# Kernel optimization log

Hardware: AMD Instinct MI355X
Metric: run time of the kernel (lower is better)

Reference implementation:

```python
import jax, jax.numpy as jnp
import numpy as np

# dims from VideoTokenizerConfig defaults + chosen video shape
B, T, IH, IW, C = 2, 16, 224, 224, 3
TP, PS, D, DFF, L, NH, K = 4, 16, 512, 2048, 6, 8, 8192
Tp, Hp, Wp = T // TP, IH // PS, IW // PS   # 4, 14, 14
S = Tp * Hp * Wp                           # 784 tokens
PIN = TP * PS * PS * C                     # 3072 patch elements
COMMIT = 0.25


def _ln(x, s, b):
    m = x.mean(-1, keepdims=True)
    v = ((x - m) ** 2).mean(-1, keepdims=True)
    return (x - m) / jnp.sqrt(v + 1e-6) * s + b


def _mha(x, Wqkv, bqkv, Wo, bo):
    b_, s_, d_ = x.shape
    hd = d_ // NH
    q = (x @ Wqkv[0] + bqkv[0]).reshape(b_, s_, NH, hd)
    k = (x @ Wqkv[1] + bqkv[1]).reshape(b_, s_, NH, hd)
    v = (x @ Wqkv[2] + bqkv[2]).reshape(b_, s_, NH, hd)
    att = jax.nn.softmax(jnp.einsum('bqhd,bkhd->bhqk', q, k) / jnp.sqrt(jnp.float32(hd)), axis=-1)
    o = jnp.einsum('bhqk,bkhd->bqhd', att, v).reshape(b_, s_, d_)
    return o @ Wo + bo


def _blocks(z, ln1s, ln1b, Wqkv, bqkv, Wo, bo, ln2s, ln2b, W1, b1, W2, b2):
    for i in range(L):  # small fixed layer count
        z = z + _mha(_ln(z, ln1s[i], ln1b[i]), Wqkv[i], bqkv[i], Wo[i], bo[i])
        h = jax.nn.gelu(_ln(z, ln2s[i], ln2b[i]) @ W1[i] + b1[i])
        z = z + h @ W2[i] + b2[i]
    return z


def _forward(video, e_patch_W, e_patch_b, e_pos_t, e_pos_h, e_pos_w,
             e_ln1_s, e_ln1_b, e_Wqkv, e_bqkv, e_Wo, e_bo, e_ln2_s, e_ln2_b,
             e_W1, e_b1, e_W2, e_b2, e_lnf_s, e_lnf_b, e_cb_W, e_cb_b,
             codebook,
             d_cb_W, d_cb_b, d_pos_t, d_pos_h, d_pos_w,
             d_ln1_s, d_ln1_b, d_Wqkv, d_bqkv, d_Wo, d_bo, d_ln2_s, d_ln2_b,
             d_W1, d_b1, d_W2, d_b2, d_lnf_s, d_lnf_b, d_px_W, d_px_b):
    # ---- encoder: 3D patchify ----
    v = video.reshape(B, Tp, TP, Hp, PS, Wp, PS, C)
    v = v.transpose(0, 1, 3, 5, 2, 4, 6, 7).reshape(B, Tp, Hp, Wp, PIN)
    z = v @ e_patch_W + e_patch_b
    z = z + e_pos_t + e_pos_h + e_pos_w
    z = z.reshape(B, S, D)
    z = _blocks(z, e_ln1_s, e_ln1_b, e_Wqkv, e_bqkv, e_Wo, e_bo,
                e_ln2_s, e_ln2_b, e_W1, e_b1, e_W2, e_b2)
    z = _ln(z, e_lnf_s, e_lnf_b)
    z_e = z @ e_cb_W + e_cb_b                      # [B,S,D]
    # ---- VQ quantize ----
    flat = z_e.reshape(-1, D)                      # [B*S, D]
    d2 = (flat ** 2).sum(1, keepdims=True) + (codebook ** 2).sum(1) - 2.0 * flat @ codebook.T
    idx = jnp.argmin(d2, axis=1)                   # [B*S]
    z_q = codebook[idx].reshape(z_e.shape)
    commit = jnp.mean((jax.lax.stop_gradient(z_q) - z_e) ** 2)
    cb_loss = jnp.mean((z_q - jax.lax.stop_gradient(z_e)) ** 2)
    z_q = z_e + jax.lax.stop_gradient(z_q - z_e)   # straight-through
    counts = jnp.zeros((K,), flat.dtype).at[idx].add(1.0)
    p = counts / idx.shape[0]                      # == mean(one_hot, axis=0)
    perplexity = jnp.exp(-jnp.sum(p * jnp.log(p + 1e-10)))
    # ---- decoder ----
    zd = z_q.reshape(B, Tp, Hp, Wp, D) @ d_cb_W + d_cb_b
    zd = zd + d_pos_t + d_pos_h + d_pos_w
    zd = zd.reshape(B, S, D)
    zd = _blocks(zd, d_ln1_s, d_ln1_b, d_Wqkv, d_bqkv, d_Wo, d_bo,
                 d_ln2_s, d_ln2_b, d_W1, d_b1, d_W2, d_b2)
    zd = _ln(zd, d_lnf_s, d_lnf_b)
    px = zd.reshape(B, Tp, Hp, Wp, D) @ d_px_W + d_px_b
    px = px.reshape(B, Tp, Hp, Wp, TP, PS, PS, C)
    recon = px.transpose(0, 1, 4, 2, 5, 3, 6, 7).reshape(B, T, IH, IW, C)
    return recon, idx.reshape(B, Tp, Hp, Wp), commit, cb_loss, perplexity


def setup_inputs() -> dict:
    key = jax.random.key(0)
    ks = iter(jax.random.split(key, 48))
    def nrm(shape, s=0.02):
        return (s * jax.random.normal(next(ks), shape)).astype(jnp.float32)
    z = lambda shape: jnp.zeros(shape, jnp.float32)
    o = lambda shape: jnp.ones(shape, jnp.float32)
    inp = {}
    inp['video'] = jax.random.normal(next(ks), (B, T, IH, IW, C), jnp.float32)
    # encoder params
    inp['e_patch_W'] = nrm((PIN, D)); inp['e_patch_b'] = z((D,))
    inp['e_pos_t'] = nrm((1, Tp, 1, 1, D)); inp['e_pos_h'] = nrm((1, 1, Hp, 1, D)); inp['e_pos_w'] = nrm((1, 1, 1, Wp, D))
    inp['e_ln1_s'] = o((L, D)); inp['e_ln1_b'] = z((L, D))
    inp['e_Wqkv'] = nrm((L, 3, D, D)); inp['e_bqkv'] = z((L, 3, D))
    inp['e_Wo'] = nrm((L, D, D)); inp['e_bo'] = z((L, D))
    inp['e_ln2_s'] = o((L, D)); inp['e_ln2_b'] = z((L, D))
    inp['e_W1'] = nrm((L, D, DFF)); inp['e_b1'] = z((L, DFF))
    inp['e_W2'] = nrm((L, DFF, D)); inp['e_b2'] = z((L, D))
    inp['e_lnf_s'] = o((D,)); inp['e_lnf_b'] = z((D,))
    inp['e_cb_W'] = nrm((D, D)); inp['e_cb_b'] = z((D,))
    inp['codebook'] = nrm((K, D))
    # decoder params
    inp['d_cb_W'] = nrm((D, D)); inp['d_cb_b'] = z((D,))
    inp['d_pos_t'] = nrm((1, Tp, 1, 1, D)); inp['d_pos_h'] = nrm((1, 1, Hp, 1, D)); inp['d_pos_w'] = nrm((1, 1, 1, Wp, D))
    inp['d_ln1_s'] = o((L, D)); inp['d_ln1_b'] = z((L, D))
    inp['d_Wqkv'] = nrm((L, 3, D, D)); inp['d_bqkv'] = z((L, 3, D))
    inp['d_Wo'] = nrm((L, D, D)); inp['d_bo'] = z((L, D))
    inp['d_ln2_s'] = o((L, D)); inp['d_ln2_b'] = z((L, D))
    inp['d_W1'] = nrm((L, D, DFF)); inp['d_b1'] = z((L, DFF))
    inp['d_W2'] = nrm((L, DFF, D)); inp['d_b2'] = z((L, D))
    inp['d_lnf_s'] = o((D,)); inp['d_lnf_b'] = z((D,))
    inp['d_px_W'] = nrm((D, PIN)); inp['d_px_b'] = z((PIN,))
    return inp


def reference(video, e_patch_W, e_patch_b, e_pos_t, e_pos_h, e_pos_w,
              e_ln1_s, e_ln1_b, e_Wqkv, e_bqkv, e_Wo, e_bo, e_ln2_s, e_ln2_b,
              e_W1, e_b1, e_W2, e_b2, e_lnf_s, e_lnf_b, e_cb_W, e_cb_b,
              codebook,
              d_cb_W, d_cb_b, d_pos_t, d_pos_h, d_pos_w,
              d_ln1_s, d_ln1_b, d_Wqkv, d_bqkv, d_Wo, d_bo, d_ln2_s, d_ln2_b,
              d_W1, d_b1, d_W2, d_b2, d_lnf_s, d_lnf_b, d_px_W, d_px_b):
    return _forward(video, e_patch_W, e_patch_b, e_pos_t, e_pos_h, e_pos_w,
                    e_ln1_s, e_ln1_b, e_Wqkv, e_bqkv, e_Wo, e_bo, e_ln2_s, e_ln2_b,
                    e_W1, e_b1, e_W2, e_b2, e_lnf_s, e_lnf_b, e_cb_W, e_cb_b,
                    codebook,
                    d_cb_W, d_cb_b, d_pos_t, d_pos_h, d_pos_w,
                    d_ln1_s, d_ln1_b, d_Wqkv, d_bqkv, d_Wo, d_bo, d_ln2_s, d_ln2_b,
                    d_W1, d_b1, d_W2, d_b2, d_lnf_s, d_lnf_b, d_px_W, d_px_b)
```

## Files before the change

### kernel.cpp

```cpp
#include <hip/hip_runtime.h>
#include <math.h>

#define Bq    2
#define Dq    512
#define DFFq  2048
#define Lq    6
#define NHq   8
#define HDq   64
#define Kq    8192
#define Sq    784
#define PINq  3072
#define TOKq  1568
#define RECN  4816896L

#define OFF_BIG  0L
#define SZ_BIG   12845056L
#define OFF_Z    (OFF_BIG + SZ_BIG)
#define OFF_XLN  (OFF_Z    + 802816L)
#define OFF_QKV  (OFF_XLN  + 802816L)
#define OFF_ATTO (OFF_QKV  + 2408448L)
#define OFF_H    (OFF_ATTO + 802816L)
#define OFF_ZE   (OFF_H    + 3211264L)
#define OFF_ZQ   (OFF_ZE   + 802816L)
#define OFF_CN   (OFF_ZQ   + 802816L)
#define OFF_IDX  (OFF_CN   + 8192L)
#define OFF_CNT  (OFF_IDX  + 1568L)
#define OFF_PART (OFF_CNT  + 8192L)
#define OFF_MIN  (OFF_PART + 1568L)
#define OFF_END  (OFF_MIN  + 3136L)

#define CEXT 802816L

typedef short bf16x8 __attribute__((ext_vector_type(8)));
typedef float f32x4  __attribute__((ext_vector_type(4)));
typedef unsigned short u16;
typedef unsigned long long u64;

#define XLO 802816L
#define QLO 2408448L
#define ALO 802816L
#define HLO 3211264L
#define PLO 4816896L
#define ZLO 802816L
#define CBLO 4194304L

__device__ __forceinline__ float wave_sum(float v) {
    #pragma unroll
    for (int o = 32; o; o >>= 1) v += __shfl_xor(v, o);
    return v;
}
__device__ __forceinline__ float gelu_f(float x) {
    float u = 0.7978845608028654f * (x + 0.044715f * x * x * x);
    float a = fabsf(u);
    float t = __expf(-2.0f * a);
    float th = (1.0f - t) / (1.0f + t);
    th = copysignf(th, u);
    return 0.5f * x * (1.0f + th);
}
__device__ __forceinline__ void split_f32(float x, u16& h, u16& l) {
    unsigned u = __float_as_uint(x);
    unsigned t = u + 0x7fffu + ((u >> 16) & 1u);
    h = (u16)(t >> 16);
    float r = x - __uint_as_float((t >> 16) << 16);
    l = (u16)(__float_as_uint(r) >> 16);
}
__device__ __forceinline__ void gload16(const u16* g, u16* l) {
    __builtin_amdgcn_global_load_lds(
        (const __attribute__((address_space(1))) void*)g,
        (__attribute__((address_space(3))) void*)l,
        16, 0, 0);
}

__global__ __launch_bounds__(256)
void wconv_t(const float* __restrict__ W, int ldw, int Kd,
             u16* __restrict__ WT, long loT, long soW, long soT)
{
    __shared__ u16 Lh[32][33], Ll[32][33];
    const float* Wp = W + (long)blockIdx.z * soW;
    u16* Tp = WT + (long)blockIdx.z * soT;
    int k0 = blockIdx.x << 5, n0 = blockIdx.y << 5;
    int t = threadIdx.x;
    int r = t >> 3, c4 = (t & 7) << 2;
    float4 v = *(const float4*)(Wp + (long)(k0 + r) * ldw + n0 + c4);
    u16 h, l;
    split_f32(v.x, h, l); Lh[c4+0][r] = h; Ll[c4+0][r] = l;
    split_f32(v.y, h, l); Lh[c4+1][r] = h; Ll[c4+1][r] = l;
    split_f32(v.z, h, l); Lh[c4+2][r] = h; Ll[c4+2][r] = l;
    split_f32(v.w, h, l); Lh[c4+3][r] = h; Ll[c4+3][r] = l;
    __syncthreads();
    int n = t >> 3, kc = (t & 7) << 2;
    u16* dst = Tp + (long)(n0 + n) * Kd + k0 + kc;
    u16 oh[4] = {Lh[n][kc], Lh[n][kc+1], Lh[n][kc+2], Lh[n][kc+3]};
    u16 ol[4] = {Ll[n][kc], Ll[n][kc+1], Ll[n][kc+2], Ll[n][kc+3]};
    *(uint2*)dst = *(uint2*)oh;
    *(uint2*)(dst + loT) = *(uint2*)ol;
}

__global__ __launch_bounds__(256)
void wconv4(const float* __restrict__ Wqkv, const float* __restrict__ Wo,
            const float* __restrict__ W1, const float* __restrict__ W2,
            u16* __restrict__ dst)
{
    __shared__ u16 Lh[32][33], Ll[32][33];
    int id = blockIdx.x;
    const float* W; int ldw, Kd, kblk, nblk; u16* Tp; long loT;
    if (id < 768) {
        int z = id >> 8, rid = id & 255;
        kblk = rid & 15; nblk = rid >> 4;
        W = Wqkv + (long)z * 262144; ldw = 512; Kd = 512;
        Tp = dst + (long)z * 262144; loT = 786432;
    } else if (id < 1024) {
        int rid = id - 768; kblk = rid & 15; nblk = rid >> 4;
        W = Wo; ldw = 512; Kd = 512; Tp = dst + 1572864; loT = 262144;
    } else if (id < 2048) {
        int rid = id - 1024; kblk = rid & 15; nblk = rid >> 4;
        W = W1; ldw = 2048; Kd = 512; Tp = dst + 2097152; loT = 1048576;
    } else {
        int rid = id - 2048; kblk = rid & 63; nblk = rid >> 6;
        W = W2; ldw = 512; Kd = 2048; Tp = dst + 4194304; loT = 1048576;
    }
    int k0 = kblk << 5, n0 = nblk << 5;
    int t = threadIdx.x;
    int r = t >> 3, c4 = (t & 7) << 2;
    float4 v = *(const float4*)(W + (long)(k0 + r) * ldw + n0 + c4);
    u16 h, l;
    split_f32(v.x, h, l); Lh[c4+0][r] = h; Ll[c4+0][r] = l;
    split_f32(v.y, h, l); Lh[c4+1][r] = h; Ll[c4+1][r] = l;
    split_f32(v.z, h, l); Lh[c4+2][r] = h; Ll[c4+2][r] = l;
    split_f32(v.w, h, l); Lh[c4+3][r] = h; Ll[c4+3][r] = l;
    __syncthreads();
    int n = t >> 3, kc = (t & 7) << 2;
    u16* d = Tp + (long)(n0 + n) * Kd + k0 + kc;
    u16 oh[4] = {Lh[n][kc], Lh[n][kc+1], Lh[n][kc+2], Lh[n][kc+3]};
    u16 ol[4] = {Ll[n][kc], Ll[n][kc+1], Ll[n][kc+2], Ll[n][kc+3]};
    *(uint2*)d = *(uint2*)oh;
    *(uint2*)(d + loT) = *(uint2*)ol;
}

__global__ __launch_bounds__(256)
void splitp(const float* __restrict__ X, u16* __restrict__ Y, long lo, long n4)
{
    long i = (long)blockIdx.x * 256 + threadIdx.x;
    if (i >= n4) return;
    float4 v = *(const float4*)(X + i * 4);
    u16 h[4], l[4];
    split_f32(v.x, h[0], l[0]); split_f32(v.y, h[1], l[1]);
    split_f32(v.z, h[2], l[2]); split_f32(v.w, h[3], l[3]);
    *(uint2*)(Y + i * 4) = *(uint2*)h;
    *(uint2*)(Y + lo + i * 4) = *(uint2*)l;
}

template<int MATH, int LV>
__global__ __launch_bounds__(256)
void gemm_bb(const u16* __restrict__ A, long rsA, long loA, long soA, long siA,
             const u16* __restrict__ B, long rsB, long loB, long soB, long siB,
             const float* __restrict__ bias, long siBias,
             const float* __restrict__ extra,
             float* __restrict__ Cf, int ldc, long soC, long siC,
             u16* __restrict__ Cb, int rsC, long loC,
             float* __restrict__ part, long pstride,
             int M, int N, int K, float alpha,
             int bdiv, int ksplit, int klen, int gx)
{
    constexpr int OFF_BH = (LV >= 2) ? 8192 : 4096;
    __shared__ u16 SH[LV == 3 ? 16384 : (LV == 2 ? 12288 : 8192)];
    const int zb2 = blockIdx.z;
    const int zk = zb2 % ksplit, zb = zb2 / ksplit;
    const int zo = zb / bdiv, zi = zb - zo * bdiv;
    A += zo * soA + zi * siA;
    B += zo * soB + zi * siB;
    const float* bi = bias ? bias + zi * siBias : nullptr;

    const int nwg = gridDim.x;
    int orig = blockIdx.x;
    int qq = nwg >> 3, rr = nwg & 7;
    int xcd = orig & 7, sidx = orig >> 3;
    int wgid = (xcd < rr ? xcd * (qq + 1) : rr * (qq + 1) + (xcd - rr) * qq) + sidx;
    const int m0 = (wgid % gx) << 6, n0 = (wgid / gx) << 6;

    const int t = threadIdx.x;
    const int kbeg = zk * klen;
    int kend = kbeg + klen; if (kend > K) kend = K;

    const int w = t >> 6, lane = t & 63;
    const int wm = w >> 1, wn = w & 1;
    const int l15 = lane & 15, g = lane >> 4;
    const int wq = w << 9;

    const int csrc = ((t & 3) + ((t >> 3) & 7)) & 3;
    int arow = m0 + (t >> 2); if (arow > M - 1) arow = M - 1;
    const u16* Apr = A + (long)arow * rsA + (csrc << 3);
    const u16* Bpr = B + (long)(n0 + (t >> 2)) * rsB + (csrc << 3);

    f32x4 acc[2][2] = {};

    for (int k0 = kbeg; k0 < kend; k0 += 64) {
        gload16(Apr + k0,            &SH[wq]);
        if (LV >= 2) gload16(Apr + k0 + loA,      &SH[4096 + wq]);
        gload16(Bpr + k0,            &SH[OFF_BH + wq]);
        if (LV == 3) gload16(Bpr + k0 + loB, &SH[12288 + wq]);
        gload16(Apr + k0 + 32,       &SH[2048 + wq]);
        if (LV >= 2) gload16(Apr + k0 + 32 + loA, &SH[4096 + 2048 + wq]);
        gload16(Bpr + k0 + 32,       &SH[OFF_BH + 2048 + wq]);
        if (LV == 3) gload16(Bpr + k0 + 32 + loB, &SH[12288 + 2048 + wq]);
        __syncthreads();

        #pragma unroll
        for (int sub = 0; sub < 2; ++sub) {
            const int so = sub << 11;
            bf16x8 ah[2], al2[2], bh2[2], bl2[2];
            #pragma unroll
            for (int mi = 0; mi < 2; ++mi) {
                int row = (wm << 5) + (mi << 4) + l15;
                int off = (row << 5) + (((g - (row >> 1)) & 3) << 3);
                ah[mi]  = *(const bf16x8*)&SH[so + off];
                if (LV >= 2) al2[mi] = *(const bf16x8*)&SH[4096 + so + off];
            }
            #pragma unroll
            for (int ni = 0; ni < 2; ++ni) {
                int row = (wn << 5) + (ni << 4) + l15;
                int off = (row << 5) + (((g - (row >> 1)) & 3) << 3);
                bh2[ni] = *(const bf16x8*)&SH[OFF_BH + so + off];
                if (LV == 3) bl2[ni] = *(const bf16x8*)&SH[12288 + so + off];
            }
            #pragma unroll
            for (int mi = 0; mi < 2; ++mi)
                #pragma unroll
                for (int ni = 0; ni < 2; ++ni) {
                    acc[mi][ni] = __builtin_amdgcn_mfma_f32_16x16x32_bf16(ah[mi], bh2[ni], acc[mi][ni], 0, 0, 0);
                    if (LV == 3) acc[mi][ni] = __builtin_amdgcn_mfma_f32_16x16x32_bf16(ah[mi], bl2[ni], acc[mi][ni], 0, 0, 0);
                    if (LV >= 2) acc[mi][ni] = __builtin_amdgcn_mfma_f32_16x16x32_bf16(al2[mi], bh2[ni], acc[mi][ni], 0, 0, 0);
                }
        }
        __syncthreads();
    }

    if (ksplit > 1) {
        float* P = part + (long)zk * pstride + zo * soC + zi * siC;
        #pragma unroll
        for (int mi = 0; mi < 2; ++mi)
            #pragma unroll
            for (int ni = 0; ni < 2; ++ni) {
                int gn = n0 + (wn << 5) + (ni << 4) + l15;
                if (gn >= N) continue;
                int gmb = m0 + (wm << 5) + (mi << 4) + (g << 2);
                #pragma unroll
                for (int r = 0; r < 4; ++r) {
                    int gm = gmb + r;
                    if (gm < M) P[(long)gm * ldc + gn] = acc[mi][ni][r];
                }
            }
        return;
    }
    if (MATH == 0) {
        float* Co = Cf + zo * soC + zi * siC;
        #pragma unroll
        for (int mi = 0; mi < 2; ++mi)
            #pragma unroll
            for (int ni = 0; ni < 2; ++ni) {
                int gn = n0 + (wn << 5) + (ni << 4) + l15;
                if (gn >= N) continue;
                int gmb = m0 + (wm << 5) + (mi << 4) + (g << 2);
                #pragma unroll
                for (int r = 0; r < 4; ++r) {
                    int gm = gmb + r;
                    if (gm >= M) continue;
                    Co[(long)gm * ldc + gn] = alpha * acc[mi][ni][r] + (bi ? bi[gn] : 0.0f);
                }
            }
    } else if (MATH == 5) {
        u64* mb = (u64*)Cf;
        #pragma unroll
        for (int mi = 0; mi < 2; ++mi) {
            #pragma unroll
            for (int r = 0; r < 4; ++r) {
                u64 best = 0xFFFFFFFFFFFFFFFFULL;
                #pragma unroll
                for (int ni = 0; ni < 2; ++ni) {
                    int gn = n0 + (wn << 5) + (ni << 4) + l15;
                    float v = extra[gn] - 2.0f * acc[mi][ni][r];
                    unsigned ub = __float_as_uint(v);
                    ub = ub ^ ((ub >> 31) ? 0xFFFFFFFFu : 0x80000000u);
                    u64 pk = ((u64)ub << 32) | (unsigned)gn;
                    best = pk < best ? pk : best;
                }
                #pragma unroll
                for (int sft = 1; sft <= 8; sft <<= 1) {
                    u64 o = __shfl_xor(best, sft);
                    best = o < best ? o : best;
                }
                if (l15 == 0) {
                    int gm = m0 + (wm << 5) + (mi << 4) + (g << 2) + r;
                    if (gm < M) atomicMin(&mb[gm], best);
                }
            }
        }
    } else {
        u16* Cu = Cb + zo * soC + zi * siC;
        #pragma unroll
        for (int mi = 0; mi < 2; ++mi)
            #pragma unroll
            for (int ni = 0; ni < 2; ++ni) {
                int gn = n0 + (wn << 5) + (ni << 4) + l15;
                if (gn >= N) continue;
                int gmb = m0 + (wm << 5) + (mi << 4) + (g << 2);
                #pragma unroll
                for (int r = 0; r < 4; ++r) {
                    int gm = gmb + r;
                    if (gm >= M) continue;
                    float v = acc[mi][ni][r] + bi[gn];
                    if (MATH == 2) v = gelu_f(v);
                    u16 h, l; split_f32(v, h, l);
                    Cu[(long)gm * rsC + gn] = h;
                    Cu[(long)gm * rsC + gn + loC] = l;
                }
            }
    }
}

#define KP 72
#define VP 40
#define CHR 196
template<bool X2>
__global__ __launch_bounds__(256)
void flash_kernel(const u16* __restrict__ qkv, float* __restrict__ O4, float* __restrict__ ML)
{
    __shared__ u16 Kh[32 * KP], Kl[32 * KP];
    __shared__ u16 Vh[64 * VP], Vl[64 * VP];
    __shared__ u16 Ph[64 * VP], Pl[64 * VP];

    const int qb = blockIdx.x, bh = blockIdx.y, ch = blockIdx.z;
    const int b = bh >> 3, h = bh & 7;
    const int jbeg = ch * CHR, jend = jbeg + CHR;
    const int t = threadIdx.x, w = t >> 6, lane = t & 63;
    const int l15 = lane & 15, g = lane >> 4;
    const long base = (long)b * 784 * 1536;
    const u16* Qg = qkv + base + h * 64;
    const u16* Kg = qkv + base + 512 + h * 64;
    const u16* Vg = qkv + base + 1024 + h * 64;

    const int q0 = qb << 6;
    int qr = q0 + w * 16 + l15; if (qr > 783) qr = 783;
    const u16* Qp = Qg + (long)qr * 1536 + g * 8;
    bf16x8 qh[2], ql[2];
    qh[0] = *(const bf16x8*)(Qp);
    qh[1] = *(const bf16x8*)(Qp + 32);
    ql[0] = *(const bf16x8*)(Qp + QLO);
    ql[1] = *(const bf16x8*)(Qp + QLO + 32);

    f32x4 O[4] = {};
    float m_[4] = {-1e30f, -1e30f, -1e30f, -1e30f};
    float l_[4] = {};

    const int srow = t >> 3, sc = (t & 7) << 3;

    for (int j0 = jbeg; j0 < jend; j0 += 32) {
        {
            int jr = j0 + srow;
            if (jr < jend) {
                const u16* Kp = Kg + (long)jr * 1536 + sc;
                *(uint4*)&Kh[srow * KP + sc] = *(const uint4*)(Kp);
                if (!X2) *(uint4*)&Kl[srow * KP + sc] = *(const uint4*)(Kp + QLO);
                const u16* Vp = Vg + (long)jr * 1536 + sc;
                u16 th[8], tl[8];
                *(uint4*)th = *(const uint4*)Vp;
                if (!X2) *(uint4*)tl = *(const uint4*)(Vp + QLO);
                #pragma unroll
                for (int e = 0; e < 8; ++e) {
                    Vh[(sc + e) * VP + srow] = th[e];
                    if (!X2) Vl[(sc + e) * VP + srow] = tl[e];
                }
            } else {
                uint4 zz = {0, 0, 0, 0};
                *(uint4*)&Kh[srow * KP + sc] = zz;
                if (!X2) *(uint4*)&Kl[srow * KP + sc] = zz;
                #pragma unroll
                for (int e = 0; e < 8; ++e) {
                    Vh[(sc + e) * VP + srow] = 0;
                    if (!X2) Vl[(sc + e) * VP + srow] = 0;
                }
            }
        }
        __syncthreads();

        f32x4 S[2] = {};
        #pragma unroll
        for (int f = 0; f < 2; ++f) {
            #pragma unroll
            for (int ks = 0; ks < 2; ++ks) {
                bf16x8 kh = *(const bf16x8*)&Kh[(f * 16 + l15) * KP + ks * 32 + g * 8];
                S[f] = __builtin_amdgcn_mfma_f32_16x16x32_bf16(qh[ks], kh, S[f], 0, 0, 0);
                if (!X2) {
                    bf16x8 kl = *(const bf16x8*)&Kl[(f * 16 + l15) * KP + ks * 32 + g * 8];
                    S[f] = __builtin_amdgcn_mfma_f32_16x16x32_bf16(qh[ks], kl, S[f], 0, 0, 0);
                }
                S[f] = __builtin_amdgcn_mfma_f32_16x16x32_bf16(ql[ks], kh, S[f], 0, 0, 0);
            }
        }

        float p[2][4];
        #pragma unroll
        for (int f = 0; f < 2; ++f) {
            bool ok = (j0 + f * 16 + l15) < jend;
            #pragma unroll
            for (int r = 0; r < 4; ++r)
                p[f][r] = ok ? S[f][r] * 0.125f : -1e30f;
        }
        #pragma unroll
        for (int r = 0; r < 4; ++r) {
            float pm = fmaxf(p[0][r], p[1][r]);
            pm = fmaxf(pm, __shfl_xor(pm, 1)); pm = fmaxf(pm, __shfl_xor(pm, 2));
            pm = fmaxf(pm, __shfl_xor(pm, 4)); pm = fmaxf(pm, __shfl_xor(pm, 8));
            float mn = fmaxf(m_[r], pm);
            float scl = __expf(m_[r] - mn);
            float rs = 0.f;
            #pragma unroll
            for (int f = 0; f < 2; ++f) { float e = __expf(p[f][r] - mn); p[f][r] = e; rs += e; }
            rs += __shfl_xor(rs, 1); rs += __shfl_xor(rs, 2);
            rs += __shfl_xor(rs, 4); rs += __shfl_xor(rs, 8);
            l_[r] = l_[r] * scl + rs;
            m_[r] = mn;
            O[0][r] *= scl; O[1][r] *= scl; O[2][r] *= scl; O[3][r] *= scl;
        }

        #pragma unroll
        for (int f = 0; f < 2; ++f)
            #pragma unroll
            for (int r = 0; r < 4; ++r) {
                u16 hh, ll; split_f32(p[f][r], hh, ll);
                int row = w * 16 + g * 4 + r;
                Ph[row * VP + f * 16 + l15] = hh;
                Pl[row * VP + f * 16 + l15] = ll;
            }

        bf16x8 pah = *(const bf16x8*)&Ph[(w * 16 + l15) * VP + g * 8];
        bf16x8 pal = *(const bf16x8*)&Pl[(w * 16 + l15) * VP + g * 8];
        #pragma unroll
        for (int f = 0; f < 4; ++f) {
            bf16x8 vh = *(const bf16x8*)&Vh[(f * 16 + l15) * VP + g * 8];
            O[f] = __builtin_amdgcn_mfma_f32_16x16x32_bf16(pah, vh, O[f], 0, 0, 0);
            O[f] = __builtin_amdgcn_mfma_f32_16x16x32_bf16(pal, vh, O[f], 0, 0, 0);
            if (!X2) {
                bf16x8 vl = *(const bf16x8*)&Vl[(f * 16 + l15) * VP + g * 8];
                O[f] = __builtin_amdgcn_mfma_f32_16x16x32_bf16(pah, vl, O[f], 0, 0, 0);
            }
        }
        __syncthreads();
    }

    #pragma unroll
    for (int r = 0; r < 4; ++r) {
        int q = q0 + w * 16 + g * 4 + r;
        if (q >= 784) continue;
        long rowi = ((long)ch * 16 + bh) * 784 + q;
        if (l15 == 0) { ML[rowi * 2] = m_[r]; ML[rowi * 2 + 1] = l_[r]; }
        #pragma unroll
        for (int f = 0; f < 4; ++f)
            O4[rowi * 64 + f * 16 + l15] = O[f][r];
    }
}

__global__ __launch_bounds__(256)
void flash_combine(const float* __restrict__ O4, const float* __restrict__ ML,
                   u16* __restrict__ atto)
{
    int wave = threadIdx.x >> 6, lane = threadIdx.x & 63;
    int row = (blockIdx.x << 2) + wave;
    int bh = row / 784, q = row - bh * 784;
    int b = bh >> 3, h = bh & 7;
    float mm[4], ll[4];
    float M = -1e30f;
    #pragma unroll
    for (int c = 0; c < 4; ++c) {
        long ri = ((long)c * 16 + bh) * 784 + q;
        mm[c] = ML[ri * 2]; ll[c] = ML[ri * 2 + 1];
        M = fmaxf(M, mm[c]);
    }
    float L = 0.f, sc[4];
    #pragma unroll
    for (int c = 0; c < 4; ++c) { sc[c] = __expf(mm[c] - M); L += sc[c] * ll[c]; }
    float o = 0.f;
    #pragma unroll
    for (int c = 0; c < 4; ++c)
        o += O4[(((long)c * 16 + bh) * 784 + q) * 64 + lane] * sc[c];
    o /= L;
    u16 hh, lo2; split_f32(o, hh, lo2);
    long off = ((long)b * 784 + q) * 512 + h * 64 + lane;
    atto[off] = hh; atto[off + ALO] = lo2;
}

template<int MATH>
__global__ __launch_bounds__(256)
void reduce_k(const float* __restrict__ part, long pstride, int ks,
              const float* __restrict__ bias, int ldc,
              float* __restrict__ Cf, u16* __restrict__ Cb, long loC, long total)
{
    long i = (long)blockIdx.x * 256 + threadIdx.x;
    if (i >= total) return;
    float s = 0.f;
    for (int k = 0; k < ks; ++k) s += part[(long)k * pstride + i];
    int col = (int)(i % ldc);
    float v = s + (bias ? bias[col] : 0.0f);
    if (MATH == 3) { Cf[i] = v; u16 h, l; split_f32(v, h, l); Cb[i] = h; Cb[i + loC] = l; }
    else { float g = gelu_f(v); u16 h, l; split_f32(g, h, l); Cb[i] = h; Cb[i + loC] = l; }
}

__global__ __launch_bounds__(256)
void redln(const float* __restrict__ part, long pstride, int ks,
           const float* __restrict__ bias,
           float* __restrict__ z,
           const float* __restrict__ s, const float* __restrict__ b,
           u16* __restrict__ y, long lo)
{
    int wave = threadIdx.x >> 6, lane = threadIdx.x & 63;
    int row = (blockIdx.x << 2) + wave;
    int c0 = lane << 3;
    long base = (long)row * 512 + c0;
    float a[8] = {};
    for (int k = 0; k < ks; ++k) {
        const float* p = part + (long)k * pstride + base;
        float4 p0 = *(const float4*)p, p1 = *(const float4*)(p + 4);
        a[0]+=p0.x; a[1]+=p0.y; a[2]+=p0.z; a[3]+=p0.w;
        a[4]+=p1.x; a[5]+=p1.y; a[6]+=p1.z; a[7]+=p1.w;
    }
    float4 b0 = *(const float4*)(bias + c0), b1 = *(const float4*)(bias + c0 + 4);
    a[0]+=b0.x; a[1]+=b0.y; a[2]+=b0.z; a[3]+=b0.w;
    a[4]+=b1.x; a[5]+=b1.y; a[6]+=b1.z; a[7]+=b1.w;
    float4 z0 = *(const float4*)(z + base), z1 = *(const float4*)(z + base + 4);
    float v[8] = { z0.x+a[0], z0.y+a[1], z0.z+a[2], z0.w+a[3],
                   z1.x+a[4], z1.y+a[5], z1.z+a[6], z1.w+a[7] };
    float4 o0, o1;
    o0.x=v[0]; o0.y=v[1]; o0.z=v[2]; o0.w=v[3];
    o1.x=v[4]; o1.y=v[5]; o1.z=v[6]; o1.w=v[7];
    *(float4*)(z + base) = o0; *(float4*)(z + base + 4) = o1;
    float sum = v[0]+v[1]+v[2]+v[3]+v[4]+v[5]+v[6]+v[7];
    sum = wave_sum(sum);
    float m = sum * (1.0f / 512.0f);
    float var = 0.f;
    float d[8];
    #pragma unroll
    for (int j = 0; j < 8; ++j) { d[j] = v[j] - m; var += d[j]*d[j]; }
    var = wave_sum(var);
    float rstd = 1.0f / sqrtf(var * (1.0f / 512.0f) + 1e-6f);
    u16 hh[8], ll[8];
    #pragma unroll
    for (int j = 0; j < 8; ++j)
        split_f32(d[j] * rstd * s[c0+j] + b[c0+j], hh[j], ll[j]);
    *(uint4*)(y + base) = *(uint4*)hh;
    *(uint4*)(y + lo + base) = *(uint4*)ll;
}

__global__ __launch_bounds__(256)
void redposln(const float* __restrict__ part, long pstride, int ks,
              const float* __restrict__ bias,
              const float* __restrict__ pt, const float* __restrict__ ph,
              const float* __restrict__ pw,
              float* __restrict__ z,
              const float* __restrict__ s, const float* __restrict__ b,
              u16* __restrict__ y, long lo)
{
    int wave = threadIdx.x >> 6, lane = threadIdx.x & 63;
    int row = (blockIdx.x << 2) + wave;
    int c0 = lane << 3;
    long base = (long)row * 512 + c0;
    int r = row % 784;
    int wp = r % 14, hh2 = (r / 14) % 14, tp = r / 196;
    float v[8] = {};
    for (int k = 0; k < ks; ++k) {
        const float* p = part + (long)k * pstride + base;
        float4 p0 = *(const float4*)p, p1 = *(const float4*)(p + 4);
        v[0]+=p0.x; v[1]+=p0.y; v[2]+=p0.z; v[3]+=p0.w;
        v[4]+=p1.x; v[5]+=p1.y; v[6]+=p1.z; v[7]+=p1.w;
    }
    const float* ptp = pt + tp * 512 + c0;
    const float* php = ph + hh2 * 512 + c0;
    const float* pwp = pw + wp * 512 + c0;
    #pragma unroll
    for (int j = 0; j < 8; ++j) v[j] += bias[c0+j] + ptp[j] + php[j] + pwp[j];
    float4 o0, o1;
    o0.x=v[0]; o0.y=v[1]; o0.z=v[2]; o0.w=v[3];
    o1.x=v[4]; o1.y=v[5]; o1.z=v[6]; o1.w=v[7];
    *(float4*)(z + base) = o0; *(float4*)(z + base + 4) = o1;
    float sum = v[0]+v[1]+v[2]+v[3]+v[4]+v[5]+v[6]+v[7];
    sum = wave_sum(sum);
    float m = sum * (1.0f / 512.0f);
    float var = 0.f; float d[8];
    #pragma unroll
    for (int j = 0; j < 8; ++j) { d[j] = v[j] - m; var += d[j]*d[j]; }
    var = wave_sum(var);
    float rstd = 1.0f / sqrtf(var * (1.0f / 512.0f) + 1e-6f);
    u16 hh[8], ll[8];
    #pragma unroll
    for (int j = 0; j < 8; ++j)
        split_f32(d[j] * rstd * s[c0+j] + b[c0+j], hh[j], ll[j]);
    *(uint4*)(y + base) = *(uint4*)hh;
    *(uint4*)(y + lo + base) = *(uint4*)ll;
}

__global__ __launch_bounds__(256)
void cnorm_kernel(const float* __restrict__ cb, float* __restrict__ cn)
{
    int wave = threadIdx.x >> 6, lane = threadIdx.x & 63;
    int row = (blockIdx.x << 2) + wave;
    if (row >= Kq) return;
    const float* cr = cb + (long)row * Dq;
    float4 v0 = *(const float4*)(cr + (lane << 2));
    float4 v1 = *(const float4*)(cr + 256 + (lane << 2));
    float ss = v0.x*v0.x+v0.y*v0.y+v0.z*v0.z+v0.w*v0.w
             + v1.x*v1.x+v1.y*v1.y+v1.z*v1.z+v1.w*v1.w;
    ss = wave_sum(ss);
    if (lane == 0) cn[row] = ss;
}

__global__ void patchify_kernel(const float* __restrict__ video, u16* __restrict__ patches)
{
    long i = (long)blockIdx.x * 256 + threadIdx.x;
    if (i >= (long)TOKq * PINq) return;
    int row = (int)(i / PINq), col = (int)(i - (long)row * PINq);
    int c = col % 3; int q = col / 3;
    int pw = q & 15; q >>= 4;
    int ph = q & 15; int tpin = q >> 4;
    int wp = row % 14; int r2 = row / 14;
    int hp = r2 % 14; r2 /= 14;
    int tp = r2 & 3; int b = r2 >> 2;
    int tt = tp * 4 + tpin;
    int ih = hp * 16 + ph, iw = wp * 16 + pw;
    float v = video[(((long)(b * 16 + tt) * 224 + ih) * 224 + iw) * 3 + c];
    u16 h, l; split_f32(v, h, l);
    patches[i] = h; patches[PLO + i] = l;
}

__global__ void unpatchify_kernel(const float* __restrict__ px, float* __restrict__ out)
{
    long o = (long)blockIdx.x * 256 + threadIdx.x;
    if (o >= RECN) return;
    int c = (int)(o % 3); long r = o / 3;
    int iw = (int)(r % 224); r /= 224;
    int ih = (int)(r % 224); r /= 224;
    int tt = (int)(r % 16); int b = (int)(r / 16);
    int tp = tt >> 2, tpin = tt & 3;
    int hp = ih >> 4, ph = ih & 15;
    int wp = iw >> 4, pw = iw & 15;
    long prow = ((long)(b * 4 + tp) * 14 + hp) * 14 + wp;
    int pcol = ((tpin * 16 + ph) * 16 + pw) * 3 + c;
    out[o] = px[prow * PINq + pcol];
}

__global__ __launch_bounds__(256)
void zq_kernel(const float* __restrict__ cb, const u64* __restrict__ minb,
               const float* __restrict__ ze, u16* __restrict__ zqp, long lo,
               float* __restrict__ part, float* __restrict__ counts,
               float* __restrict__ out_idx)
{
    int tok = blockIdx.x;
    int id = (int)(minb[tok] & 0xFFFFFFFFULL);
    const float* c = cb + (long)id * Dq;
    const float* z = ze + (long)tok * Dq;
    float ss = 0.f;
    for (int d = threadIdx.x; d < Dq; d += 256) {
        float cv = c[d];
        u16 h, l; split_f32(cv, h, l);
        zqp[(long)tok * Dq + d] = h;
        zqp[lo + (long)tok * Dq + d] = l;
        float df = cv - z[d];
        ss += df * df;
    }
    float wsum = wave_sum(ss);
    __shared__ float sw[4];
    if ((threadIdx.x & 63) == 0) sw[threadIdx.x >> 6] = wsum;
    __syncthreads();
    if (threadIdx.x == 0) {
        part[tok] = sw[0] + sw[1] + sw[2] + sw[3];
        atomicAdd(&counts[id], 1.0f);
        out_idx[tok] = (float)id;
    }
}

__global__ __launch_bounds__(256)
void scalars_kernel(const float* __restrict__ part, const float* __restrict__ counts,
                    float* __restrict__ out)
{
    float se = 0.f;
    for (int t = threadIdx.x; t < TOKq; t += 256) se += part[t];
    float pl = 0.f;
    for (int k = threadIdx.x; k < Kq; k += 256) {
        float p = counts[k] * (1.0f / 1568.0f);
        pl += p * logf(p + 1e-10f);
    }
    float wse = wave_sum(se), wpl = wave_sum(pl);
    __shared__ float s1[4], s2[4];
    if ((threadIdx.x & 63) == 0) { s1[threadIdx.x >> 6] = wse; s2[threadIdx.x >> 6] = wpl; }
    __syncthreads();
    if (threadIdx.x == 0) {
        float sse = s1[0] + s1[1] + s1[2] + s1[3];
        float plo = s2[0] + s2[1] + s2[2] + s2[3];
        float commit = sse / 802816.0f;
        out[RECN + 1568 + 0] = commit;
        out[RECN + 1568 + 1] = commit;
        out[RECN + 1568 + 2] = expf(-plo);
    }
}

template<int LVA, int LVF, bool FX2>
static void block_fwd(hipStream_t st, float* z, float* big, float* hbuf,
                      u16* xlnu, u16* qkvu, u16* attou, u16* hbu, u16* wscr,
                      const float* Wqkv, const float* bqkv,
                      const float* Wo, const float* bo,
                      const float* ln2s, const float* ln2b,
                      const float* W1, const float* b1,
                      const float* W2, const float* b2,
                      const float* nls, const float* nlb)
{
    wconv4<<<3072, 256, 0, st>>>(Wqkv, Wo, W1, W2, wscr);
    gemm_bb<4, LVA><<<dim3(600, 1, 1), 256, 0, st>>>(
        xlnu, Dq, XLO, 0, 0,
        wscr, Dq, 786432, 0, 0,
        bqkv, 0, nullptr,
        nullptr, 0, 0, 0,
        qkvu, 1536, QLO,
        nullptr, 0,
        TOKq, 1536, Dq, 1.0f, 1, 1, Dq, 25);
    flash_kernel<FX2><<<dim3(13, 16, 4), 256, 0, st>>>(qkvu, big, big + 3211264L);
    flash_combine<<<3136, 256, 0, st>>>(big, big + 3211264L, attou);
    gemm_bb<0, LVA><<<dim3(200, 1, 4), 256, 0, st>>>(
        attou, Dq, ALO, 0, 0,
        wscr + 1572864, Dq, 262144, 0, 0,
        nullptr, 0, nullptr,
        nullptr, Dq, 0, 0,
        nullptr, 0, 0,
        hbuf, CEXT,
        TOKq, Dq, Dq, 1.0f, 1, 4, 128, 25);
    redln<<<392, 256, 0, st>>>(hbuf, CEXT, 4, bo, z, ln2s, ln2b, xlnu, XLO);
    gemm_bb<2, LVF><<<dim3(800, 1, 1), 256, 0, st>>>(
        xlnu, Dq, XLO, 0, 0,
        wscr + 2097152, Dq, 1048576, 0, 0,
        b1, 0, nullptr,
        nullptr, 0, 0, 0,
        hbu, DFFq, HLO,
        nullptr, 0,
        TOKq, DFFq, Dq, 1.0f, 1, 1, Dq, 25);
    gemm_bb<0, LVF><<<dim3(200, 1, 4), 256, 0, st>>>(
        hbu, DFFq, HLO, 0, 0,
        wscr + 4194304, DFFq, 1048576, 0, 0,
        nullptr, 0, nullptr,
        nullptr, Dq, 0, 0,
        nullptr, 0, 0,
        big, CEXT,
        TOKq, Dq, DFFq, 1.0f, 1, 4, 512, 25);
    redln<<<392, 256, 0, st>>>(big, CEXT, 4, b2, z, nls, nlb, xlnu, XLO);
}

extern "C" void kernel_launch(void* const* d_in, const int* in_sizes, int n_in,
                              void* d_out, int out_size, void* d_ws, size_t ws_size,
                              hipStream_t stream)
{
    (void)in_sizes; (void)n_in; (void)out_size;
    if (ws_size < (size_t)OFF_END * sizeof(float)) return;

    const float* video = (const float*)d_in[0];
    const float* epW   = (const float*)d_in[1];  const float* epb   = (const float*)d_in[2];
    const float* ept   = (const float*)d_in[3];  const float* ephp  = (const float*)d_in[4];
    const float* epwp  = (const float*)d_in[5];
    const float* eln1s = (const float*)d_in[6];  const float* eln1b = (const float*)d_in[7];
    const float* eWqkv = (const float*)d_in[8];  const float* ebqkv = (const float*)d_in[9];
    const float* eWo   = (const float*)d_in[10]; const float* ebo   = (const float*)d_in[11];
    const float* eln2s = (const float*)d_in[12]; const float* eln2b = (const float*)d_in[13];
    const float* eW1   = (const float*)d_in[14]; const float* eb1   = (const float*)d_in[15];
    const float* eW2   = (const float*)d_in[16]; const float* eb2   = (const float*)d_in[17];
    const float* elnfs = (const float*)d_in[18]; const float* elnfb = (const float*)d_in[19];
    const float* ecbW  = (const float*)d_in[20]; const float* ecbb  = (const float*)d_in[21];
    const float* cbook = (const float*)d_in[22];
    const float* dcbW  = (const float*)d_in[23]; const float* dcbb  = (const float*)d_in[24];
    const float* dpt   = (const float*)d_in[25]; const float* dphp  = (const float*)d_in[26];
    const float* dpwp  = (const float*)d_in[27];
    const float* dln1s = (const float*)d_in[28]; const float* dln1b = (const float*)d_in[29];
    const float* dWqkv = (const float*)d_in[30]; const float* dbqkv = (const float*)d_in[31];
    const float* dWo   = (const float*)d_in[32]; const float* dbo   = (const float*)d_in[33];
    const float* dln2s = (const float*)d_in[34]; const float* dln2b = (const float*)d_in[35];
    const float* dW1   = (const float*)d_in[36]; const float* db1   = (const float*)d_in[37];
    const float* dW2   = (const float*)d_in[38]; const float* db2   = (const float*)d_in[39];
    const float* dlnfs = (const float*)d_in[40]; const float* dlnfb = (const float*)d_in[41];
    const float* dpxW  = (const float*)d_in[42]; const float* dpxb  = (const float*)d_in[43];

    float* ws   = (float*)d_ws;
    float* big  = ws + OFF_BIG;
    float* z    = ws + OFF_Z;
    float* xln  = ws + OFF_XLN;
    float* qkv  = ws + OFF_QKV;
    float* atto = ws + OFF_ATTO;
    float* hbuf = ws + OFF_H;
    float* ze   = ws + OFF_ZE;
    float* zq   = ws + OFF_ZQ;
    float* cn   = ws + OFF_CN;
    float* cnt  = ws + OFF_CNT;
    float* part = ws + OFF_PART;
    u64*   minb = (u64*)(ws + OFF_MIN);
    float* out  = (float*)d_out;

    u16* xlnu  = (u16*)xln;
    u16* qkvu  = (u16*)qkv;
    u16* attou = (u16*)atto;
    u16* hbu   = (u16*)hbuf;
    u16* patu  = (u16*)big;
    u16* zqu   = (u16*)zq;
    u16* cbs   = (u16*)qkv;
    u16* wscr  = (u16*)(big + 9633792);

    hipMemsetAsync(cnt, 0, Kq * sizeof(float), stream);
    hipMemsetAsync(minb, 0xFF, TOKq * sizeof(u64), stream);
    cnorm_kernel<<<Kq / 4, 256, 0, stream>>>(cbook, cn);

    patchify_kernel<<<(int)(((long)TOKq * PINq + 255) / 256), 256, 0, stream>>>(video, patu);
    wconv_t<<<dim3(96, 16, 1), 256, 0, stream>>>(epW, Dq, PINq, wscr, 1572864, 0, 0);
    gemm_bb<0, 3><<<dim3(200, 1, 6), 256, 0, stream>>>(
        patu, PINq, PLO, 0, 0,
        wscr, PINq, 1572864, 0, 0,
        nullptr, 0, nullptr,
        nullptr, Dq, 0, 0,
        nullptr, 0, 0,
        big + PLO, CEXT,
        TOKq, Dq, PINq, 1.0f, 1, 6, 512, 25);
    redposln<<<392, 256, 0, stream>>>(big + PLO, CEXT, 6, epb, ept, ephp, epwp,
                                      z, eln1s, eln1b, xlnu, XLO);

    for (int l = 0; l < Lq; ++l) {
        const float* nls = (l < 5) ? eln1s + (l + 1) * Dq : elnfs;
        const float* nlb = (l < 5) ? eln1b + (l + 1) * Dq : elnfb;
        block_fwd<3, 3, false>(stream, z, big, hbuf, xlnu, qkvu, attou, hbu, wscr,
                         eWqkv + (long)l * 3 * Dq * Dq, ebqkv + l * 3 * Dq,
                         eWo + (long)l * Dq * Dq, ebo + l * Dq,
                         eln2s + l * Dq, eln2b + l * Dq,
                         eW1 + (long)l * Dq * DFFq, eb1 + l * DFFq,
                         eW2 + (long)l * DFFq * Dq, eb2 + l * Dq,
                         nls, nlb);
    }

    wconv_t<<<dim3(16, 16, 1), 256, 0, stream>>>(ecbW, Dq, Dq, wscr, 262144, 0, 0);
    gemm_bb<0, 3><<<dim3(200, 1, 2), 256, 0, stream>>>(
        xlnu, Dq, XLO, 0, 0,
        wscr, Dq, 262144, 0, 0,
        nullptr, 0, nullptr,
        nullptr, Dq, 0, 0,
        nullptr, 0, 0,
        big, CEXT,
        TOKq, Dq, Dq, 1.0f, 1, 2, 256, 25);
    reduce_k<3><<<(CEXT + 255) / 256, 256, 0, stream>>>(big, CEXT, 2, ecbb, Dq, ze, zqu, ZLO, CEXT);

    splitp<<<(int)(((long)Kq * Dq / 4 + 255) / 256), 256, 0, stream>>>(cbook, cbs, CBLO, (long)Kq * Dq / 4);
    gemm_bb<5, 3><<<dim3(3200, 1, 1), 256, 0, stream>>>(
        zqu, Dq, ZLO, 0, 0,
        cbs, Dq, CBLO, 0, 0,
        nullptr, 0, cn,
        (float*)minb, Kq, 0, 0,
        nullptr, 0, 0,
        nullptr, 0,
        TOKq, Kq, Dq, 1.0f, 1, 1, Dq, 25);
    zq_kernel<<<TOKq, 256, 0, stream>>>(cbook, minb, ze, zqu, ZLO, part, cnt, out + RECN);
    scalars_kernel<<<1, 256, 0, stream>>>(part, cnt, out);

    wconv_t<<<dim3(16, 16, 1), 256, 0, stream>>>(dcbW, Dq, Dq, wscr, 262144, 0, 0);
    gemm_bb<0, 2><<<dim3(200, 1, 2), 256, 0, stream>>>(
        zqu, Dq, ZLO, 0, 0,
        wscr, Dq, 262144, 0, 0,
        nullptr, 0, nullptr,
        nullptr, Dq, 0, 0,
        nullptr, 0, 0,
        big, CEXT,
        TOKq, Dq, Dq, 1.0f, 1, 2, 256, 25);
    redposln<<<392, 256, 0, stream>>>(big, CEXT, 2, dcbb, dpt, dphp, dpwp,
                                      z, dln1s, dln1b, xlnu, XLO);

    for (int l = 0; l < Lq; ++l) {
        const float* nls = (l < 5) ? dln1s + (l + 1) * Dq : dlnfs;
        const float* nlb = (l < 5) ? dln1b + (l + 1) * Dq : dlnfb;
        block_fwd<2, 1, true>(stream, z, big, hbuf, xlnu, qkvu, attou, hbu, wscr,
                        dWqkv + (long)l * 3 * Dq * Dq, dbqkv + l * 3 * Dq,
                        dWo + (long)l * Dq * Dq, dbo + l * Dq,
                        dln2s + l * Dq, dln2b + l * Dq,
                        dW1 + (long)l * Dq * DFFq, db1 + l * DFFq,
                        dW2 + (long)l * DFFq * Dq, db2 + l * Dq,
                        nls, nlb);
    }

    wconv_t<<<dim3(16, 96, 1), 256, 0, stream>>>(dpxW, PINq, Dq, wscr, 1572864, 0, 0);
    gemm_bb<0, 2><<<dim3(1200, 1, 1), 256, 0, stream>>>(
        xlnu, Dq, XLO, 0, 0,
        wscr, Dq, 1572864, 0, 0,
        dpxb, 0, nullptr,
        big, PINq, 0, 0,
        nullptr, 0, 0,
        nullptr, 0,
        TOKq, PINq, Dq, 1.0f, 1, 1, Dq, 25);
    unpatchify_kernel<<<(int)((RECN + 255) / 256), 256, 0, stream>>>(big, out);
}
```

Measured before the change: 1.703 ms.

## Add wider-tile VQ distance GEMM kernel and double flash-attention KV splits

Replaces the generic GEMM's argmin epilogue path with a dedicated kernel for the codebook distance search. It uses 64x128 tiles, so each block covers twice as many codewords, and keeps the XCD-aware block remap. This halves the grid and the number of atomicMin operations per row, and raises B-tile reuse of the loaded A tile. Flash attention also splits the key range into 8 chunks instead of 4, giving more parallel blocks, at the cost of more partial outputs for the combine kernel to read.

```diff
diff --git a/kernel.cpp b/kernel.cpp
--- a/kernel.cpp
+++ b/kernel.cpp
@@ -268,33 +268,6 @@
                     Co[(long)gm * ldc + gn] = alpha * acc[mi][ni][r] + (bi ? bi[gn] : 0.0f);
                 }
             }
-    } else if (MATH == 5) {
-        u64* mb = (u64*)Cf;
-        #pragma unroll
-        for (int mi = 0; mi < 2; ++mi) {
-            #pragma unroll
-            for (int r = 0; r < 4; ++r) {
-                u64 best = 0xFFFFFFFFFFFFFFFFULL;
-                #pragma unroll
-                for (int ni = 0; ni < 2; ++ni) {
-                    int gn = n0 + (wn << 5) + (ni << 4) + l15;
-                    float v = extra[gn] - 2.0f * acc[mi][ni][r];
-                    unsigned ub = __float_as_uint(v);
-                    ub = ub ^ ((ub >> 31) ? 0xFFFFFFFFu : 0x80000000u);
-                    u64 pk = ((u64)ub << 32) | (unsigned)gn;
-                    best = pk < best ? pk : best;
-                }
-                #pragma unroll
-                for (int sft = 1; sft <= 8; sft <<= 1) {
-                    u64 o = __shfl_xor(best, sft);
-                    best = o < best ? o : best;
-                }
-                if (l15 == 0) {
-                    int gm = m0 + (wm << 5) + (mi << 4) + (g << 2) + r;
-                    if (gm < M) atomicMin(&mb[gm], best);
-                }
-            }
-        }
     } else {
         u16* Cu = Cb + zo * soC + zi * siC;
         #pragma unroll
@@ -318,9 +291,110 @@
     }
 }
 
+__global__ __launch_bounds__(256)
+void gemm_d2w(const u16* __restrict__ A, long rsA, long loA,
+              const u16* __restrict__ B, long rsB, long loB,
+              const float* __restrict__ extra, u64* __restrict__ mb,
+              int M, int N, int K, int gx)
+{
+    __shared__ u16 SH[24576];
+    const int nwg = gridDim.x;
+    int orig = blockIdx.x;
+    int qq = nwg >> 3, rr = nwg & 7;
+    int xcd = orig & 7, sidx = orig >> 3;
+    int wgid = (xcd < rr ? xcd * (qq + 1) : rr * (qq + 1) + (xcd - rr) * qq) + sidx;
+    const int m0 = (wgid % gx) << 6, n0 = (wgid / gx) << 7;
+
+    const int t = threadIdx.x;
+    const int w = t >> 6, lane = t & 63;
+    const int wm = w >> 1, wn = w & 1;
+    const int l15 = lane & 15, g = lane >> 4;
+    const int wq = w << 9;
+
+    const int csrc = ((t & 3) + ((t >> 3) & 7)) & 3;
+    int arow = m0 + (t >> 2); if (arow > M - 1) arow = M - 1;
+    const u16* Apr = A + (long)arow * rsA + (csrc << 3);
+    const u16* Bpr0 = B + (long)(n0 + (t >> 2)) * rsB + (csrc << 3);
+    const u16* Bpr1 = B + (long)(n0 + 64 + (t >> 2)) * rsB + (csrc << 3);
+
+    f32x4 acc[2][4] = {};
+
+    for (int k0 = 0; k0 < K; k0 += 64) {
+        gload16(Apr + k0,             &SH[wq]);
+        gload16(Apr + k0 + 32,        &SH[2048 + wq]);
+        gload16(Apr + k0 + loA,       &SH[4096 + wq]);
+        gload16(Apr + k0 + 32 + loA,  &SH[4096 + 2048 + wq]);
+        gload16(Bpr0 + k0,            &SH[8192 + wq]);
+        gload16(Bpr1 + k0,            &SH[8192 + 2048 + wq]);
+        gload16(Bpr0 + k0 + 32,       &SH[12288 + wq]);
+        gload16(Bpr1 + k0 + 32,       &SH[12288 + 2048 + wq]);
+        gload16(Bpr0 + k0 + loB,      &SH[16384 + wq]);
+        gload16(Bpr1 + k0 + loB,      &SH[16384 + 2048 + wq]);
+        gload16(Bpr0 + k0 + 32 + loB, &SH[20480 + wq]);
+        gload16(Bpr1 + k0 + 32 + loB, &SH[20480 + 2048 + wq]);
+        __syncthreads();
+
+        #pragma unroll
+        for (int sub = 0; sub < 2; ++sub) {
+            const int soA = sub << 11;
+            const int soB = sub << 12;
+            bf16x8 ah[2], al2[2], bh2[4], bl2[4];
+            #pragma unroll
+            for (int mi = 0; mi < 2; ++mi) {
+                int row = (wm << 5) + (mi << 4) + l15;
+                int off = (row << 5) + (((g - (row >> 1)) & 3) << 3);
+                ah[mi]  = *(const bf16x8*)&SH[soA + off];
+                al2[mi] = *(const bf16x8*)&SH[4096 + soA + off];
+            }
+            #pragma unroll
+            for (int ni = 0; ni < 4; ++ni) {
+                int row = (wn << 6) + (ni << 4) + l15;
+                int off = (row << 5) + (((g - (row >> 1)) & 3) << 3);
+                bh2[ni] = *(const bf16x8*)&SH[8192 + soB + off];
+                bl2[ni] = *(const bf16x8*)&SH[16384 + soB + off];
+            }
+            #pragma unroll
+            for (int mi = 0; mi < 2; ++mi)
+                #pragma unroll
+                for (int ni = 0; ni < 4; ++ni) {
+                    acc[mi][ni] = __builtin_amdgcn_mfma_f32_16x16x32_bf16(ah[mi],  bh2[ni], acc[mi][ni], 0, 0, 0);
+                    acc[mi][ni] = __builtin_amdgcn_mfma_f32_16x16x32_bf16(ah[mi],  bl2[ni], acc[mi][ni], 0, 0, 0);
+                    acc[mi][ni] = __builtin_amdgcn_mfma_f32_16x16x32_bf16(al2[mi], bh2[ni], acc[mi][ni], 0, 0, 0);
+                }
+        }
+        __syncthreads();
+    }
+
+    #pragma unroll
+    for (int mi = 0; mi < 2; ++mi) {
+        #pragma unroll
+        for (int r = 0; r < 4; ++r) {
+            u64 best = 0xFFFFFFFFFFFFFFFFULL;
+            #pragma unroll
+            for (int ni = 0; ni < 4; ++ni) {
+                int gn = n0 + (wn << 6) + (ni << 4) + l15;
+                float v = extra[gn] - 2.0f * acc[mi][ni][r];
+                unsigned ub = __float_as_uint(v);
+                ub = ub ^ ((ub >> 31) ? 0xFFFFFFFFu : 0x80000000u);
+                u64 pk = ((u64)ub << 32) | (unsigned)gn;
+                best = pk < best ? pk : best;
+            }
+            #pragma unroll
+            for (int sft = 1; sft <= 8; sft <<= 1) {
+                u64 o = __shfl_xor(best, sft);
+                best = o < best ? o : best;
+            }
+            if (l15 == 0) {
+                int gm = m0 + (wm << 5) + (mi << 4) + (g << 2) + r;
+                if (gm < M) atomicMin(&mb[gm], best);
+            }
+        }
+    }
+}
+
 #define KP 72
 #define VP 40
-#define CHR 196
+#define CHR 98
 template<bool X2>
 __global__ __launch_bounds__(256)
 void flash_kernel(const u16* __restrict__ qkv, float* __restrict__ O4, float* __restrict__ ML)
@@ -468,20 +542,20 @@
     int row = (blockIdx.x << 2) + wave;
     int bh = row / 784, q = row - bh * 784;
     int b = bh >> 3, h = bh & 7;
-    float mm[4], ll[4];
+    float mm[8], ll[8];
     float M = -1e30f;
     #pragma unroll
-    for (int c = 0; c < 4; ++c) {
+    for (int c = 0; c < 8; ++c) {
         long ri = ((long)c * 16 + bh) * 784 + q;
         mm[c] = ML[ri * 2]; ll[c] = ML[ri * 2 + 1];
         M = fmaxf(M, mm[c]);
     }
-    float L = 0.f, sc[4];
-    #pragma unroll
-    for (int c = 0; c < 4; ++c) { sc[c] = __expf(mm[c] - M); L += sc[c] * ll[c]; }
+    float L = 0.f, sc[8];
+    #pragma unroll
+    for (int c = 0; c < 8; ++c) { sc[c] = __expf(mm[c] - M); L += sc[c] * ll[c]; }
     float o = 0.f;
     #pragma unroll
-    for (int c = 0; c < 4; ++c)
+    for (int c = 0; c < 8; ++c)
         o += O4[(((long)c * 16 + bh) * 784 + q) * 64 + lane] * sc[c];
     o /= L;
     u16 hh, lo2; split_f32(o, hh, lo2);
@@ -720,8 +794,8 @@
         qkvu, 1536, QLO,
         nullptr, 0,
         TOKq, 1536, Dq, 1.0f, 1, 1, Dq, 25);
-    flash_kernel<FX2><<<dim3(13, 16, 4), 256, 0, st>>>(qkvu, big, big + 3211264L);
-    flash_combine<<<3136, 256, 0, st>>>(big, big + 3211264L, attou);
+    flash_kernel<FX2><<<dim3(13, 16, 8), 256, 0, st>>>(qkvu, big, big + 6422528L);
+    flash_combine<<<3136, 256, 0, st>>>(big, big + 6422528L, attou);
     gemm_bb<0, LVA><<<dim3(200, 1, 4), 256, 0, st>>>(
         attou, Dq, ALO, 0, 0,
         wscr + 1572864, Dq, 262144, 0, 0,
@@ -847,14 +921,11 @@
     reduce_k<3><<<(CEXT + 255) / 256, 256, 0, stream>>>(big, CEXT, 2, ecbb, Dq, ze, zqu, ZLO, CEXT);
 
     splitp<<<(int)(((long)Kq * Dq / 4 + 255) / 256), 256, 0, stream>>>(cbook, cbs, CBLO, (long)Kq * Dq / 4);
-    gemm_bb<5, 3><<<dim3(3200, 1, 1), 256, 0, stream>>>(
-        zqu, Dq, ZLO, 0, 0,
-        cbs, Dq, CBLO, 0, 0,
-        nullptr, 0, cn,
-        (float*)minb, Kq, 0, 0,
-        nullptr, 0, 0,
-        nullptr, 0,
-        TOKq, Kq, Dq, 1.0f, 1, 1, Dq, 25);
+    gemm_d2w<<<dim3(1600, 1, 1), 256, 0, stream>>>(
+        zqu, Dq, ZLO,
+        cbs, Dq, CBLO,
+        cn, minb,
+        TOKq, Kq, Dq, 25);
     zq_kernel<<<TOKq, 256, 0, stream>>>(cbook, minb, ze, zqu, ZLO, part, cnt, out + RECN);
     scalars_kernel<<<1, 256, 0, stream>>>(part, cnt, out);
 
```

Measured after the change: 1.718 ms. No clear change (+0.9%).
